# Performance work log

Hardware: AMD Instinct MI355X
Metric: run time of the kernel (lower is better)

## Reference

```python
import jax, jax.numpy as jnp
import numpy as np

BSZ, SEQ, T, ENC, HID = 32, 2048, 32, 512, 512


def setup_inputs() -> dict:
    key = jax.random.key(0)
    ks = jax.random.split(key, 8)
    L = SEQ // T  # uniform turn length -> end ids cover every token
    end_ids = jnp.broadcast_to((jnp.arange(T, dtype=jnp.int32) + 1) * L - 1, (BSZ, T))
    s = 1.0 / np.sqrt(HID)
    return {
        "encoder_output": jax.random.normal(ks[0], (BSZ, SEQ, ENC), jnp.float32),
        "end_ids": end_ids,
        "W_ih": jax.random.uniform(ks[1], (4 * HID, ENC), jnp.float32, -s, s),
        "W_hh": jax.random.uniform(ks[2], (4 * HID, HID), jnp.float32, -s, s),
        "b_ih": jax.random.uniform(ks[3], (4 * HID,), jnp.float32, -s, s),
        "b_hh": jax.random.uniform(ks[4], (4 * HID,), jnp.float32, -s, s),
        "fc_w": jax.random.uniform(ks[5], (1, HID + ENC), jnp.float32, -s, s),
        "fc_b": jnp.zeros((1,), jnp.float32),
    }


def reference(encoder_output, end_ids, W_ih, W_hh, b_ih, b_hh, fc_w, fc_b):
    bsz, S, E = encoder_output.shape
    Tn = end_ids.shape[1]
    H = W_hh.shape[1]

    # ---- ragged segment-mean pooling: token t in turn j iff prev_end < t <= end[j]
    tok = jnp.arange(S)
    seg = jax.vmap(lambda e: jnp.searchsorted(e, tok))(end_ids)  # [bsz,S]
    gid = (seg + jnp.arange(bsz)[:, None] * Tn).reshape(-1)
    sums = jax.ops.segment_sum(encoder_output.reshape(-1, E), gid, num_segments=bsz * Tn)
    starts = jnp.concatenate([jnp.zeros((bsz, 1), end_ids.dtype), end_ids[:, :-1] + 1], axis=1)
    counts = (end_ids - starts + 1).astype(encoder_output.dtype)  # [bsz,Tn]
    turn_states = sums.reshape(bsz, Tn, E) / counts[..., None]

    # ---- all sliding windows of 3 consecutive turns
    J = Tn - 3
    widx = jnp.arange(J)[:, None] + jnp.arange(3)[None, :]  # [J,3]
    src = turn_states[:, widx].reshape(bsz * J, 3, E)  # [N,3,E]

    # ---- single-layer LSTM (pytorch gate order i,f,g,o), take last hidden state
    bias = b_ih + b_hh

    def step(carry, x_t):
        h, c = carry
        g = x_t @ W_ih.T + h @ W_hh.T + bias
        i_, f_, g_, o_ = jnp.split(g, 4, axis=-1)
        c = jax.nn.sigmoid(f_) * c + jax.nn.sigmoid(i_) * jnp.tanh(g_)
        h = jax.nn.sigmoid(o_) * jnp.tanh(c)
        return (h, c), None

    h0 = jnp.zeros((bsz * J, H), src.dtype)
    (hT, _), _ = jax.lax.scan(step, (h0, h0), jnp.swapaxes(src, 0, 1))

    # ---- con_fc([src_last, tgt]) decomposes into src-part + tgt-part of the weight
    sscore = (hT @ fc_w[0, :H]).reshape(bsz, J)  # [bsz,J]
    tscore = turn_states @ fc_w[0, H:]  # [bsz,Tn]
    kidx = jnp.arange(J)[:, None] + 3 + jnp.arange(J)[None, :]  # [J,J] candidate turn ids
    valid = kidx < Tn
    kc = jnp.clip(kidx, 0, Tn - 1)
    logits = sscore[:, :, None] + tscore[:, kc] + fc_b[0]  # [bsz,J,J]
    logits = jnp.where(valid[None], logits, jnp.float32(-1e9))
    # cross entropy with target index 0 (the j+3 turn is the positive)
    loss = jax.nn.logsumexp(logits, axis=-1) - logits[..., 0]  # [bsz,J]
    return jnp.mean(loss)
```

## Files before the change

### kernel.cpp

```cpp
#include <hip/hip_runtime.h>
#include <math.h>

#define BSZ   32
#define SEQL  2048
#define TN    32
#define ENCD  512
#define HIDD  512
#define JW    29
#define NW    (BSZ * JW)

typedef short bf16x8 __attribute__((ext_vector_type(8)));
typedef float f32x4  __attribute__((ext_vector_type(4)));

__device__ __forceinline__ float sigm(float x) { return 1.f / (1.f + expf(-x)); }

__device__ __forceinline__ unsigned short f2bf(float x) {
    union { float f; unsigned u; } v; v.f = x;
    unsigned u = v.u;
    u += 0x7FFF + ((u >> 16) & 1);
    return (unsigned short)(u >> 16);
}
__device__ __forceinline__ float bf2f(short s) {
    union { unsigned u; float f; } v; v.u = ((unsigned)(unsigned short)s) << 16;
    return v.f;
}

#define GLOAD_LDS16(gp, lp)                                                    \
    __builtin_amdgcn_global_load_lds(                                          \
        (const __attribute__((address_space(1))) void*)(gp),                   \
        (__attribute__((address_space(3))) void*)(lp), 16, 0, 0)

__global__ __launch_bounds__(512) void prep_k(const float* __restrict__ enc,
                                              const int* __restrict__ end_ids,
                                              short* __restrict__ tsbf,
                                              const float* __restrict__ w1,
                                              const float* __restrict__ w2,
                                              short* __restrict__ o1,
                                              short* __restrict__ o2,
                                              const float* __restrict__ fcw,
                                              float* __restrict__ tsc) {
    int tid = threadIdx.x;
    int bid = blockIdx.x;
    if (bid >= 1024) {
        int idx = (bid - 1024) * 512 + tid;
        int t = idx >> 17;
        int i = idx & 131071;
        const float* s = (t ? w2 : w1) + (size_t)i * 8;
        short* o = (t ? o2 : o1) + (size_t)i * 8;
        float4 a = ((const float4*)s)[0];
        float4 b = ((const float4*)s)[1];
        union { short v[8]; bf16x8 p; } r;
        r.v[0] = (short)f2bf(a.x); r.v[1] = (short)f2bf(a.y);
        r.v[2] = (short)f2bf(a.z); r.v[3] = (short)f2bf(a.w);
        r.v[4] = (short)f2bf(b.x); r.v[5] = (short)f2bf(b.y);
        r.v[6] = (short)f2bf(b.z); r.v[7] = (short)f2bf(b.w);
        *(bf16x8*)o = r.p;
        return;
    }
    int j = bid & 31;
    int b = bid >> 5;
    int e_end   = end_ids[bid];
    int e_start = j ? (end_ids[bid - 1] + 1) : 0;
    int col = (tid & 127) << 2;
    int tr  = tid >> 7;
    const float* base = enc + (size_t)b * SEQL * ENCD + col;
    float ax = 0.f, ay = 0.f, az = 0.f, aw = 0.f;
    float bx = 0.f, by = 0.f, bz = 0.f, bw = 0.f;
    for (int t = e_start + tr; t <= e_end; t += 8) {
        float4 v = *(const float4*)(base + (size_t)t * ENCD);
        ax += v.x; ay += v.y; az += v.z; aw += v.w;
        int t2 = t + 4;
        if (t2 <= e_end) {
            float4 u = *(const float4*)(base + (size_t)t2 * ENCD);
            bx += u.x; by += u.y; bz += u.z; bw += u.w;
        }
    }
    ax += bx; ay += by; az += bz; aw += bw;
    __shared__ float4 part[3][128];
    __shared__ float red[128];
    if (tr) part[tr - 1][tid & 127] = make_float4(ax, ay, az, aw);
    __syncthreads();
    if (!tr) {
        float4 p0 = part[0][tid], p1 = part[1][tid], p2 = part[2][tid];
        float inv = 1.f / (float)(e_end - e_start + 1);
        float mx = (ax + p0.x + p1.x + p2.x) * inv;
        float my = (ay + p0.y + p1.y + p2.y) * inv;
        float mz = (az + p0.z + p1.z + p2.z) * inv;
        float mw = (aw + p0.w + p1.w + p2.w) * inv;
        union { unsigned short v[4]; uint2 p; } q;
        q.v[0] = f2bf(mx); q.v[1] = f2bf(my); q.v[2] = f2bf(mz); q.v[3] = f2bf(mw);
        *(uint2*)(tsbf + (size_t)bid * ENCD + col) = q.p;
        float4 wv = *(const float4*)(fcw + HIDD + col);
        red[tid] = mx * wv.x + my * wv.y + mz * wv.z + mw * wv.w;
    }
    __syncthreads();
    if (tid < 64) {
        float s = red[tid] + red[tid + 64];
#pragma unroll
        for (int sh = 32; sh; sh >>= 1) s += __shfl_down(s, sh, 64);
        if (tid == 0) tsc[bid] = s;
    }
}

template <int STEP>
__global__ __launch_bounds__(128) void gemm_lstm(const short* __restrict__ A,
                                                 const short* __restrict__ B,
                                                 ushort4* __restrict__ XWq,
                                                 float* __restrict__ Cb,
                                                 short* __restrict__ Hout,
                                                 float* __restrict__ ss_part,
                                                 const float* __restrict__ b_ih,
                                                 const float* __restrict__ b_hh,
                                                 const float* __restrict__ fcw) {
    __shared__ short Als[2][2 * 512];
    __shared__ short Bls[2][16 * 512];
    int tid = threadIdx.x, w = tid >> 6, lane = tid & 63;
    int l15 = lane & 15, l4 = lane >> 4;
    int m0 = blockIdx.y * 16, hcol0 = blockIdx.x * 32;
    int hcol = hcol0 + w * 16 + l15;
    const short* Aptr = A + (size_t)m0 * 512;
    f32x4 acc[4] = {};

    auto stage = [&](int sel, int k0) {
#pragma unroll
        for (int i = 0; i < 9; ++i) {
            int c = w * 9 + i;
            if (c < 2) {
                int unit = c * 64 + lane;
                int row = unit >> 3, slot = unit & 7;
                int scol = slot ^ (row & 7);
                GLOAD_LDS16(Aptr + (size_t)row * 512 + k0 + scol * 8,
                            &Als[sel][c * 512]);
            } else {
                int cc = c - 2;
                int unit = cc * 64 + lane;
                int rr = unit >> 3, slot = unit & 7;
                int grow = (rr >> 5) * 512 + hcol0 + (rr & 31);
                int scol = slot ^ (rr & 7);
                GLOAD_LDS16(B + (size_t)grow * 512 + k0 + scol * 8,
                            &Bls[sel][cc * 512]);
            }
        }
    };

    stage(0, 0);
    __syncthreads();
    int sel = 0;
    for (int t = 0; t < 8; ++t) {
        if (t < 7) stage(sel ^ 1, (t + 1) * 64);
        bf16x8 af[2], bfr[4][2];
#pragma unroll
        for (int kk = 0; kk < 2; ++kk) {
            int row = l15;
            int s = (kk * 4 + l4) ^ (row & 7);
            af[kk] = *(const bf16x8*)&Als[sel][row * 64 + s * 8];
#pragma unroll
            for (int g = 0; g < 4; ++g) {
                int rr = g * 32 + w * 16 + l15;
                int s2 = (kk * 4 + l4) ^ (rr & 7);
                bfr[g][kk] = *(const bf16x8*)&Bls[sel][rr * 64 + s2 * 8];
            }
        }
#pragma unroll
        for (int kk = 0; kk < 2; ++kk)
#pragma unroll
            for (int g = 0; g < 4; ++g)
                acc[g] = __builtin_amdgcn_mfma_f32_16x16x32_bf16(
                    af[kk], bfr[g][kk], acc[g], 0, 0, 0);
        __syncthreads();
        sel ^= 1;
    }

    float bb0, bb1, bb2, bb3;
    if (STEP == 1) {
        bb0 = b_ih[hcol]        + b_hh[hcol];
        bb1 = b_ih[512 + hcol]  + b_hh[512 + hcol];
        bb2 = b_ih[1024 + hcol] + b_hh[1024 + hcol];
        bb3 = b_ih[1536 + hcol] + b_hh[1536 + hcol];
    }
    float hreg[4];
#pragma unroll
    for (int r = 0; r < 4; ++r) {
        int row = m0 + l4 * 4 + r;
        float gi = acc[0][r], gf = acc[1][r];
        float gg = acc[2][r], go = acc[3][r];
        float cn;
        if (STEP == 1) {
            gi += bb0; gf += bb1; gg += bb2; go += bb3;
            ushort4 q;
            q.x = f2bf(gi); q.y = f2bf(gf); q.z = f2bf(gg); q.w = f2bf(go);
            XWq[(size_t)row * 512 + hcol] = q;
            cn = sigm(gi) * tanhf(gg);
        } else {
            int xr = row + (STEP - 1); if (xr > 1023) xr = 1023;
            ushort4 q = XWq[(size_t)xr * 512 + hcol];
            gi += bf2f((short)q.x); gf += bf2f((short)q.y);
            gg += bf2f((short)q.z); go += bf2f((short)q.w);
            cn = sigm(gf) * Cb[(size_t)row * 512 + hcol] + sigm(gi) * tanhf(gg);
        }
        float h = sigm(go) * tanhf(cn);
        if (STEP < 3) {
            Cb[(size_t)row * 512 + hcol] = cn;
            Hout[(size_t)row * 512 + hcol] = (short)f2bf(h);
        } else {
            hreg[r] = h;
        }
    }
    if (STEP == 3) {
        float fcv = fcw[hcol];
        float* sred = (float*)&Als[0][0];
        float vals[4];
#pragma unroll
        for (int r = 0; r < 4; ++r) {
            float v = hreg[r] * fcv;
#pragma unroll
            for (int m = 1; m < 16; m <<= 1) v += __shfl_xor(v, m, 64);
            vals[r] = v;
        }
        __syncthreads();
        if (w == 0 && l15 == 0)
#pragma unroll
            for (int r = 0; r < 4; ++r) sred[l4 * 4 + r] = vals[r];
        __syncthreads();
        if (w == 1 && l15 == 0)
#pragma unroll
            for (int r = 0; r < 4; ++r) sred[l4 * 4 + r] += vals[r];
        __syncthreads();
        if (tid < 16) ss_part[(size_t)(m0 + tid) * 16 + blockIdx.x] = sred[tid];
    }
}

__global__ __launch_bounds__(1024) void loss_k(const float* __restrict__ ss_part,
                                               const float* __restrict__ tsc,
                                               const float* __restrict__ fcb,
                                               float* __restrict__ out) {
    int tid = threadIdx.x;
    float l = 0.f;
    if (tid < NW) {
        int b = tid / JW, j = tid - (tid / JW) * JW;
        int turn = b * TN + j;
        const float* sp = ss_part + (size_t)turn * 16;
        float s = 0.f;
#pragma unroll
        for (int k = 0; k < 16; ++k) s += sp[k];
        float base = s + fcb[0];
        int nv = JW - j;
        const float* tp = tsc + b * TN + j + 3;
        float m = -1e30f, l0 = 0.f;
        for (int k = 0; k < nv; ++k) {
            float lg = base + tp[k];
            if (k == 0) l0 = lg;
            m = fmaxf(m, lg);
        }
        float sum = 0.f;
        for (int k = 0; k < nv; ++k) sum += expf(base + tp[k] - m);
        l = (m + logf(sum)) - l0;
    }
    __shared__ float red[16];
#pragma unroll
    for (int s = 32; s; s >>= 1) l += __shfl_down(l, s, 64);
    int wid = tid >> 6, lane = tid & 63;
    if (lane == 0) red[wid] = l;
    __syncthreads();
    if (tid == 0) {
        float tot = 0.f;
        for (int i = 0; i < 16; ++i) tot += red[i];
        out[0] = tot / (float)NW;
    }
}

extern "C" void kernel_launch(void* const* d_in, const int* in_sizes, int n_in,
                              void* d_out, int out_size, void* d_ws, size_t ws_size,
                              hipStream_t stream) {
    const float* enc     = (const float*)d_in[0];
    const int*   end_ids = (const int*)d_in[1];
    const float* W_ih    = (const float*)d_in[2];
    const float* W_hh    = (const float*)d_in[3];
    const float* b_ih    = (const float*)d_in[4];
    const float* b_hh    = (const float*)d_in[5];
    const float* fc_w    = (const float*)d_in[6];
    const float* fc_b    = (const float*)d_in[7];
    float* out = (float*)d_out;

    short* tsbf   = (short*)d_ws;
    short* Wih_bf = tsbf + 1024 * 512;
    short* Whh_bf = Wih_bf + 2048 * 512;
    short* HA     = Whh_bf + 2048 * 512;
    short* HB     = HA + 1024 * 512;
    ushort4* XWq  = (ushort4*)(HB + 1024 * 512);
    float* Cb     = (float*)(XWq + 1024 * 512);
    float* ss_part = Cb + 1024 * 512;
    float* tsc    = ss_part + 1024 * 16;

    prep_k<<<1536, 512, 0, stream>>>(enc, end_ids, tsbf, W_ih, W_hh,
                                     Wih_bf, Whh_bf, fc_w, tsc);
    gemm_lstm<1><<<dim3(16, 64), 128, 0, stream>>>(tsbf, Wih_bf, XWq, Cb, HA,
                                                   nullptr, b_ih, b_hh, fc_w);
    gemm_lstm<2><<<dim3(16, 64), 128, 0, stream>>>(HA, Whh_bf, XWq, Cb, HB,
                                                   nullptr, b_ih, b_hh, fc_w);
    gemm_lstm<3><<<dim3(16, 64), 128, 0, stream>>>(HB, Whh_bf, XWq, Cb, nullptr,
                                                   ss_part, b_ih, b_hh, fc_w);
    loss_k<<<1, 1024, 0, stream>>>(ss_part, tsc, fc_b, out);
}
```

Measured before the change: 68.55 us.

## Retile LSTM GEMM with full-K weight panel resident in LDS

Each block now loads a full-K 64x512 slice of the gate weights into shared memory once and streams only activation tiles in double buffers. Blocks are 256 threads covering 64 rows by 16 hidden columns instead of 16 rows by 32 columns. This cuts repeated weight staging per k-step and per-block redundant weight traffic, and the final fc reduction now writes per-wave partials directly, which doubles the partial count summed in the loss kernel. The trade is a 64KB+ LDS footprint per block, which limits occupancy and leaves fewer blocks (512) in the grid.

```diff
diff --git a/kernel.cpp b/kernel.cpp
--- a/kernel.cpp
+++ b/kernel.cpp
@@ -103,7 +103,7 @@
 }
 
 template <int STEP>
-__global__ __launch_bounds__(128) void gemm_lstm(const short* __restrict__ A,
+__global__ __launch_bounds__(256, 2) void gemm_lstm(const short* __restrict__ A,
                                                  const short* __restrict__ B,
                                                  ushort4* __restrict__ XWq,
                                                  float* __restrict__ Cb,
@@ -112,53 +112,50 @@
                                                  const float* __restrict__ b_ih,
                                                  const float* __restrict__ b_hh,
                                                  const float* __restrict__ fcw) {
-    __shared__ short Als[2][2 * 512];
-    __shared__ short Bls[2][16 * 512];
+    __shared__ short Bpanel[64 * 512];
+    __shared__ short Als[2][64 * 64];
     int tid = threadIdx.x, w = tid >> 6, lane = tid & 63;
     int l15 = lane & 15, l4 = lane >> 4;
-    int m0 = blockIdx.y * 16, hcol0 = blockIdx.x * 32;
-    int hcol = hcol0 + w * 16 + l15;
+    int m0 = blockIdx.y * 64, hcol0 = blockIdx.x * 16;
+    int hcol = hcol0 + l15;
     const short* Aptr = A + (size_t)m0 * 512;
+
+#pragma unroll
+    for (int i = 0; i < 16; ++i) {
+        int r = w * 16 + i;
+        int grow = (r >> 4) * 512 + hcol0 + (r & 15);
+        int scol = lane ^ (r & 7);
+        GLOAD_LDS16(B + (size_t)grow * 512 + scol * 8, &Bpanel[r * 512]);
+    }
+    auto stageA = [&](int sel, int k0) {
+#pragma unroll
+        for (int i = 0; i < 2; ++i) {
+            int c = w * 2 + i;
+            int unit = c * 64 + lane;
+            int row = unit >> 3, slot = unit & 7;
+            int scol = slot ^ (row & 7);
+            GLOAD_LDS16(Aptr + (size_t)row * 512 + k0 + scol * 8,
+                        &Als[sel][c * 512]);
+        }
+    };
+    stageA(0, 0);
+    __syncthreads();
+
     f32x4 acc[4] = {};
-
-    auto stage = [&](int sel, int k0) {
-#pragma unroll
-        for (int i = 0; i < 9; ++i) {
-            int c = w * 9 + i;
-            if (c < 2) {
-                int unit = c * 64 + lane;
-                int row = unit >> 3, slot = unit & 7;
-                int scol = slot ^ (row & 7);
-                GLOAD_LDS16(Aptr + (size_t)row * 512 + k0 + scol * 8,
-                            &Als[sel][c * 512]);
-            } else {
-                int cc = c - 2;
-                int unit = cc * 64 + lane;
-                int rr = unit >> 3, slot = unit & 7;
-                int grow = (rr >> 5) * 512 + hcol0 + (rr & 31);
-                int scol = slot ^ (rr & 7);
-                GLOAD_LDS16(B + (size_t)grow * 512 + k0 + scol * 8,
-                            &Bls[sel][cc * 512]);
-            }
-        }
-    };
-
-    stage(0, 0);
-    __syncthreads();
     int sel = 0;
     for (int t = 0; t < 8; ++t) {
-        if (t < 7) stage(sel ^ 1, (t + 1) * 64);
+        if (t < 7) stageA(sel ^ 1, (t + 1) * 64);
         bf16x8 af[2], bfr[4][2];
 #pragma unroll
         for (int kk = 0; kk < 2; ++kk) {
-            int row = l15;
+            int row = w * 16 + l15;
             int s = (kk * 4 + l4) ^ (row & 7);
             af[kk] = *(const bf16x8*)&Als[sel][row * 64 + s * 8];
 #pragma unroll
             for (int g = 0; g < 4; ++g) {
-                int rr = g * 32 + w * 16 + l15;
-                int s2 = (kk * 4 + l4) ^ (rr & 7);
-                bfr[g][kk] = *(const bf16x8*)&Bls[sel][rr * 64 + s2 * 8];
+                int rr = g * 16 + l15;
+                int s2 = t * 8 + ((kk * 4 + l4) ^ (rr & 7));
+                bfr[g][kk] = *(const bf16x8*)&Bpanel[rr * 512 + s2 * 8];
             }
         }
 #pragma unroll
@@ -181,7 +178,7 @@
     float hreg[4];
 #pragma unroll
     for (int r = 0; r < 4; ++r) {
-        int row = m0 + l4 * 4 + r;
+        int row = m0 + w * 16 + l4 * 4 + r;
         float gi = acc[0][r], gf = acc[1][r];
         float gg = acc[2][r], go = acc[3][r];
         float cn;
@@ -208,25 +205,16 @@
     }
     if (STEP == 3) {
         float fcv = fcw[hcol];
-        float* sred = (float*)&Als[0][0];
-        float vals[4];
 #pragma unroll
         for (int r = 0; r < 4; ++r) {
             float v = hreg[r] * fcv;
 #pragma unroll
             for (int m = 1; m < 16; m <<= 1) v += __shfl_xor(v, m, 64);
-            vals[r] = v;
-        }
-        __syncthreads();
-        if (w == 0 && l15 == 0)
-#pragma unroll
-            for (int r = 0; r < 4; ++r) sred[l4 * 4 + r] = vals[r];
-        __syncthreads();
-        if (w == 1 && l15 == 0)
-#pragma unroll
-            for (int r = 0; r < 4; ++r) sred[l4 * 4 + r] += vals[r];
-        __syncthreads();
-        if (tid < 16) ss_part[(size_t)(m0 + tid) * 16 + blockIdx.x] = sred[tid];
+            if (l15 == 0) {
+                int row = m0 + w * 16 + l4 * 4 + r;
+                ss_part[(size_t)row * 32 + blockIdx.x] = v;
+            }
+        }
     }
 }
 
@@ -239,10 +227,10 @@
     if (tid < NW) {
         int b = tid / JW, j = tid - (tid / JW) * JW;
         int turn = b * TN + j;
-        const float* sp = ss_part + (size_t)turn * 16;
+        const float* sp = ss_part + (size_t)turn * 32;
         float s = 0.f;
 #pragma unroll
-        for (int k = 0; k < 16; ++k) s += sp[k];
+        for (int k = 0; k < 32; ++k) s += sp[k];
         float base = s + fcb[0];
         int nv = JW - j;
         const float* tp = tsc + b * TN + j + 3;
@@ -290,15 +278,15 @@
     ushort4* XWq  = (ushort4*)(HB + 1024 * 512);
     float* Cb     = (float*)(XWq + 1024 * 512);
     float* ss_part = Cb + 1024 * 512;
-    float* tsc    = ss_part + 1024 * 16;
+    float* tsc    = ss_part + 1024 * 32;
 
     prep_k<<<1536, 512, 0, stream>>>(enc, end_ids, tsbf, W_ih, W_hh,
                                      Wih_bf, Whh_bf, fc_w, tsc);
-    gemm_lstm<1><<<dim3(16, 64), 128, 0, stream>>>(tsbf, Wih_bf, XWq, Cb, HA,
+    gemm_lstm<1><<<dim3(32, 16), 256, 0, stream>>>(tsbf, Wih_bf, XWq, Cb, HA,
                                                    nullptr, b_ih, b_hh, fc_w);
-    gemm_lstm<2><<<dim3(16, 64), 128, 0, stream>>>(HA, Whh_bf, XWq, Cb, HB,
+    gemm_lstm<2><<<dim3(32, 16), 256, 0, stream>>>(HA, Whh_bf, XWq, Cb, HB,
                                                    nullptr, b_ih, b_hh, fc_w);
-    gemm_lstm<3><<<dim3(16, 64), 128, 0, stream>>>(HB, Whh_bf, XWq, Cb, nullptr,
+    gemm_lstm<3><<<dim3(32, 16), 256, 0, stream>>>(HB, Whh_bf, XWq, Cb, nullptr,
                                                    ss_part, b_ih, b_hh, fc_w);
     loss_k<<<1, 1024, 0, stream>>>(ss_part, tsc, fc_b, out);
 }
```

New measurement: 67.51 us. Within noise of the previous version (-1.5%).
